# Kernel tuning notes

Measured on AMD Instinct MI355X. Metric: run time of the kernel, lower is better.

## Reference

```python
import jax, jax.numpy as jnp
import numpy as np

T, B, I, H = 512, 128, 512, 1024


def setup_inputs() -> dict:
    key = jax.random.key(0)
    ks = jax.random.split(key, 9)
    stdv = 1.0 / np.sqrt(H).astype(np.float32)
    u = lambda k, shape: jax.random.uniform(k, shape, jnp.float32, -stdv, stdv)
    return {
        "x": jax.random.normal(ks[0], (T, B, I), jnp.float32),
        "Wf": u(ks[1], (H, H + I)), "bf": u(ks[2], (H,)),
        "Wi": u(ks[3], (H, H + I)), "bi": u(ks[4], (H,)),
        "Wc": u(ks[5], (H, H + I)), "bc": u(ks[6], (H,)),
        "Wo": u(ks[7], (H, H + I)), "bo": u(ks[8], (H,)),
    }


def reference(x, Wf, bf, Wi, bi, Wc, bc, Wo, bo):
    # Single-layer unidirectional LSTM (colah equations), scan over time.
    hidden = Wf.shape[0]
    batch = x.shape[1]

    def step(carry, xt):
        h, c = carry
        z = jnp.concatenate([h, xt], axis=-1)          # (B, H+I)
        f = jax.nn.sigmoid(z @ Wf.T + bf)              # forget gate
        i = jax.nn.sigmoid(z @ Wi.T + bi)              # input gate
        c_tilde = jnp.tanh(z @ Wc.T + bc)              # candidate cell
        o = jax.nn.sigmoid(z @ Wo.T + bo)              # output gate
        c_new = f * c + i * c_tilde
        h_new = o * jnp.tanh(c_new)
        return (h_new, c_new), h_new

    h0 = jnp.zeros((batch, hidden), x.dtype)
    c0 = jnp.zeros((batch, hidden), x.dtype)
    (_, _), hs = jax.lax.scan(step, (h0, c0), x)       # hs: (T, B, H)
    return hs
```

## Files before the change

### kernel.cpp

```cpp
#include <hip/hip_runtime.h>
#include <hip/hip_fp16.h>

#define TSTEPS 512
#define NB 128
#define NI 512
#define HID 1024
#define NWGS 256

typedef _Float16 __attribute__((ext_vector_type(8))) half8;
typedef float __attribute__((ext_vector_type(16))) floatx16;
typedef float __attribute__((ext_vector_type(4))) float4v;
typedef unsigned __attribute__((ext_vector_type(4))) uint4v;

#define WPACK_OFF 0
#define HB0_OFF   12582912
#define HB1_OFF   12845056
#define BAR_OFF   13107200

#define LDS_PBUF  98304
#define LDS_HSH   135168
#define LDS_TOTAL 137728

__device__ __forceinline__ short f2h(float f) {
  _Float16 h = (_Float16)f;
  return *reinterpret_cast<short*>(&h);
}

__device__ __forceinline__ half8 pack8(float4v a, float4v b) {
  half8 r;
  r[0] = (_Float16)a[0]; r[1] = (_Float16)a[1]; r[2] = (_Float16)a[2]; r[3] = (_Float16)a[3];
  r[4] = (_Float16)b[0]; r[5] = (_Float16)b[1]; r[6] = (_Float16)b[2]; r[7] = (_Float16)b[3];
  return r;
}

__device__ __forceinline__ float sigf(float x) { return 1.f / (1.f + __expf(-x)); }

__device__ __forceinline__ uint4v cp_load4(const unsigned* p) {
  uint4v v;
  asm volatile("global_load_dwordx4 %0, %1, off sc0 sc1" : "=v"(v) : "v"(p) : "memory");
  asm volatile("s_waitcnt vmcnt(0)" ::: "memory");
  return v;
}
__device__ __forceinline__ void cp_store(unsigned* p, unsigned v) {
  asm volatile("global_store_dword %0, %1, off sc0 sc1" :: "v"(p), "v"(v) : "memory");
}

__global__ void pack_w(const float* __restrict__ Wf, const float* __restrict__ Wi,
                       const float* __restrict__ Wc, const float* __restrict__ Wo,
                       _Float16* __restrict__ wpack) {
  int idx = blockIdx.x * 256 + threadIdx.x;
  if (idx >= 128 * 96 * 64) return;
  int lane = idx & 63;
  int rest = idx >> 6;
  int kt = rest % 96;
  int hs = rest / 96;
  int n = lane & 31, q = lane >> 5;
  int j = n >> 2, g = n & 3;
  int row = hs * 8 + j;
  int k = kt * 16 + q * 8;
  const float* W = (g == 0) ? Wf : (g == 1) ? Wi : (g == 2) ? Wc : Wo;
  const float* src = W + (size_t)row * 1536 + k;
  _Float16* dst = wpack + (size_t)idx * 8;
  #pragma unroll
  for (int e = 0; e < 8; e++) dst[e] = (_Float16)src[e];
}

__global__ void zero_h(unsigned* __restrict__ hb0, unsigned* __restrict__ bar) {
  int i = blockIdx.x * 256 + threadIdx.x;
  if (i < 65536)
    __hip_atomic_store(&hb0[i], 0u, __ATOMIC_RELAXED, __HIP_MEMORY_SCOPE_SYSTEM);
  if (i < 512)
    __hip_atomic_store(&bar[i], 0u, __ATOMIC_RELAXED, __HIP_MEMORY_SCOPE_SYSTEM);
}

__global__ void __launch_bounds__(256, 1)
lstm_main(const float* __restrict__ x,
          const float* __restrict__ bfv, const float* __restrict__ biv,
          const float* __restrict__ bcv, const float* __restrict__ bov,
          const _Float16* __restrict__ wpack,
          _Float16* __restrict__ hb0, _Float16* __restrict__ hb1,
          unsigned* __restrict__ bar, float* __restrict__ out) {
  extern __shared__ char lds[];
  short* wlds = (short*)lds;
  float* pbuf = (float*)(lds + LDS_PBUF);
  float* hshare = (float*)(lds + LDS_HSH);

  const int tid = threadIdx.x;
  const int lane = tid & 63;
  const int wv = tid >> 6;
  const int hs = blockIdx.x & 127;
  const int mh = blockIdx.x >> 7;

  {
    const uint4* src = (const uint4*)wpack + (size_t)hs * 6144;
    uint4* dst = (uint4*)wlds;
    #pragma unroll
    for (int i = 0; i < 24; i++) dst[i * 256 + tid] = src[i * 256 + tid];
  }

  const int rj = tid & 7;
  const int rm4 = tid >> 3;
  float rbias[4] = {0.f, 0.f, 0.f, 0.f};
  float cstate[4] = {0.f, 0.f, 0.f, 0.f};
  if (tid < 128) {
    int hg = hs * 8 + rj;
    rbias[0] = bfv[hg]; rbias[1] = biv[hg]; rbias[2] = bcv[hg]; rbias[3] = bov[hg];
  }

  const int n32 = lane & 31;
  const int q = lane >> 5;

  __syncthreads();

  for (int t = 0; t < TSTEPS; t++) {
    const _Float16* hrd = (t & 1) ? hb1 : hb0;
    _Float16* hwr = (t & 1) ? hb0 : hb1;

    floatx16 acc0, acc1;
    #pragma unroll
    for (int i = 0; i < 16; i++) { acc0[i] = 0.f; acc1[i] = 0.f; }

    {
      const float* xbase = x + (size_t)t * NB * NI;
      const int r0 = (mh * 2 + 0) * 32 + n32;
      #pragma unroll
      for (int kk = 0; kk < 8; kk++) {
        int xt = wv * 8 + kk;
        half8 bfrag = *(const half8*)(wlds + ((64 + xt) * 64 + lane) * 8);
        const float* xs = xbase + xt * 16 + q * 8;
        float4v xa0 = *(const float4v*)(xs + (size_t)r0 * NI);
        float4v xb0 = *(const float4v*)(xs + (size_t)r0 * NI + 4);
        float4v xa1 = *(const float4v*)(xs + (size_t)(r0 + 32) * NI);
        float4v xb1 = *(const float4v*)(xs + (size_t)(r0 + 32) * NI + 4);
        acc0 = __builtin_amdgcn_mfma_f32_32x32x16_f16(pack8(xa0, xb0), bfrag, acc0, 0, 0, 0);
        acc1 = __builtin_amdgcn_mfma_f32_32x32x16_f16(pack8(xa1, xb1), bfrag, acc1, 0, 0, 0);
      }
    }

    if (t > 0) {
      const unsigned need = (unsigned)t;
      if (tid < 32) {
        const unsigned* p = bar + mh * 128 + tid * 4;
        for (;;) {
          uint4v v = cp_load4(p);
          int ok = (v[0] >= need) & (v[1] >= need) & (v[2] >= need) & (v[3] >= need);
          unsigned long long b = __ballot(ok);
          if ((unsigned)b == 0xFFFFFFFFu) break;
          __builtin_amdgcn_s_sleep(2);
        }
      }
      __syncthreads();
    }

    {
      const char* hp = (const char*)hrd + ((size_t)mh << 17);
      #pragma unroll
      for (int ph = 0; ph < 2; ph++) {
        uint4v wa[8], wb[8];
        #pragma unroll
        for (int kk = 0; kk < 8; kk++) {
          int ht = wv * 16 + ph * 8 + kk;
          const char* base = hp + (((ht * 2 + q) << 10) | (n32 << 4));
          asm volatile("global_load_dwordx4 %0, %1, off sc0 sc1"
                       : "=v"(wa[kk]) : "v"(base));
          asm volatile("global_load_dwordx4 %0, %1, off offset:512 sc0 sc1"
                       : "=v"(wb[kk]) : "v"(base));
        }
        #pragma unroll
        for (int kk = 0; kk < 8; kk++) {
          int ht = wv * 16 + ph * 8 + kk;
          half8 bfrag = *(const half8*)(wlds + (ht * 64 + lane) * 8);
          asm volatile("s_waitcnt vmcnt(%0)" :: "i"(14 - 2 * kk) : "memory");
          __builtin_amdgcn_sched_barrier(0);
          union { uint4v u; half8 h; } ua, ub;
          ua.u = wa[kk]; ub.u = wb[kk];
          acc0 = __builtin_amdgcn_mfma_f32_32x32x16_f16(ua.h, bfrag, acc0, 0, 0, 0);
          acc1 = __builtin_amdgcn_mfma_f32_32x32x16_f16(ub.h, bfrag, acc1, 0, 0, 0);
        }
      }
    }

    {
      float* b0 = pbuf + ((wv * 2 + 0) * 32 + n32) * 36 + q * 4;
      float* b1 = pbuf + ((wv * 2 + 1) * 32 + n32) * 36 + q * 4;
      #pragma unroll
      for (int rg = 0; rg < 4; rg++) {
        float4v v0 = {acc0[rg * 4 + 0], acc0[rg * 4 + 1], acc0[rg * 4 + 2], acc0[rg * 4 + 3]};
        float4v v1 = {acc1[rg * 4 + 0], acc1[rg * 4 + 1], acc1[rg * 4 + 2], acc1[rg * 4 + 3]};
        *(float4v*)(b0 + rg * 8) = v0;
        *(float4v*)(b1 + rg * 8) = v1;
      }
    }
    __syncthreads();

    if (tid < 128) {
      const int mt = rm4 >> 3;
      const int mb = (rm4 & 7) * 4;
      float4v s[4];
      #pragma unroll
      for (int g = 0; g < 4; g++) {
        const float* p = pbuf + (mt * 32 + rj * 4 + g) * 36 + mb;
        float4v a = *(const float4v*)(p);
        a += *(const float4v*)(p + 1 * 2 * 32 * 36);
        a += *(const float4v*)(p + 2 * 2 * 32 * 36);
        a += *(const float4v*)(p + 3 * 2 * 32 * 36);
        s[g] = a;
      }
      #pragma unroll
      for (int r = 0; r < 4; r++) {
        float fg = sigf(s[0][r] + rbias[0]);
        float ig = sigf(s[1][r] + rbias[1]);
        float cg = tanhf(s[2][r] + rbias[2]);
        float og = sigf(s[3][r] + rbias[3]);
        float cn = fg * cstate[r] + ig * cg;
        cstate[r] = cn;
        hshare[(rm4 * 4 + r) * 10 + rj] = og * tanhf(cn);
      }
    }
    __syncthreads();

    {
      const int ml = tid >> 2;
      const int j0 = (tid & 3) * 2;
      float h0 = hshare[ml * 10 + j0];
      float h1 = hshare[ml * 10 + j0 + 1];

      unsigned u = ((unsigned)(unsigned short)f2h(h1) << 16) | (unsigned)(unsigned short)f2h(h0);
      unsigned* dst = (unsigned*)((char*)hwr + (((mh * 128 + hs) << 10))) + tid;
      cp_store(dst, u);

      const int mg = mh * 64 + ml;
      const int hg = hs * 8 + j0;
      *(float2*)(out + ((size_t)t * NB + mg) * HID + hg) = make_float2(h0, h1);
    }

    if (t < TSTEPS - 1) {
      __syncthreads();
      if (tid == 0) {
        asm volatile("s_waitcnt vmcnt(0)" ::: "memory");
        cp_store(&bar[blockIdx.x], (unsigned)(t + 1));
      }
    }
  }
}

extern "C" void kernel_launch(void* const* d_in, const int* in_sizes, int n_in,
                              void* d_out, int out_size, void* d_ws, size_t ws_size,
                              hipStream_t stream) {
  const float* x   = (const float*)d_in[0];
  const float* Wf  = (const float*)d_in[1];
  const float* bf_ = (const float*)d_in[2];
  const float* Wi  = (const float*)d_in[3];
  const float* bi_ = (const float*)d_in[4];
  const float* Wc  = (const float*)d_in[5];
  const float* bc_ = (const float*)d_in[6];
  const float* Wo  = (const float*)d_in[7];
  const float* bo_ = (const float*)d_in[8];
  float* out = (float*)d_out;

  char* ws = (char*)d_ws;
  _Float16* wpack = (_Float16*)(ws + WPACK_OFF);
  _Float16* hb0   = (_Float16*)(ws + HB0_OFF);
  _Float16* hb1   = (_Float16*)(ws + HB1_OFF);
  unsigned* bar   = (unsigned*)(ws + BAR_OFF);

  pack_w<<<3072, 256, 0, stream>>>(Wf, Wi, Wc, Wo, wpack);
  zero_h<<<257, 256, 0, stream>>>((unsigned*)hb0, bar);

  hipFuncSetAttribute(reinterpret_cast<const void*>(lstm_main),
                      hipFuncAttributeMaxDynamicSharedMemorySize, LDS_TOTAL);

  void* args[] = {(void*)&x, (void*)&bf_, (void*)&bi_, (void*)&bc_, (void*)&bo_,
                  (void*)&wpack, (void*)&hb0, (void*)&hb1, (void*)&bar, (void*)&out};
  hipLaunchCooperativeKernel(reinterpret_cast<void*>(lstm_main),
                             dim3(NWGS), dim3(256), args, LDS_TOTAL, stream);
}
```

Before: 4.210 ms.

## Drop LDS h staging, skip zero-h matmul at t=0, defer output stores

The gate-math threads now pair adjacent hidden values with a lane shuffle and write the fp16 recurrent state straight to global memory. This removes the LDS hshare buffer and one workgroup barrier per timestep. The h-recurrent MFMA pass now runs only for t>0, so the kernel no longer needs to zero the initial h buffer. The fp32 output stores are issued after the barrier flag is published, so they overlap with other workgroups' waiting. The explicit vmcnt wait before the flag store is gone, so correctness now depends on the barrier's memory fence ordering the h stores before the flag.

```diff
diff --git a/kernel.cpp b/kernel.cpp
--- a/kernel.cpp
+++ b/kernel.cpp
@@ -18,8 +18,7 @@
 #define BAR_OFF   13107200
 
 #define LDS_PBUF  98304
-#define LDS_HSH   135168
-#define LDS_TOTAL 137728
+#define LDS_TOTAL 135168
 
 __device__ __forceinline__ short f2h(float f) {
   _Float16 h = (_Float16)f;
@@ -65,10 +64,8 @@
   for (int e = 0; e < 8; e++) dst[e] = (_Float16)src[e];
 }
 
-__global__ void zero_h(unsigned* __restrict__ hb0, unsigned* __restrict__ bar) {
+__global__ void zero_bar(unsigned* __restrict__ bar) {
   int i = blockIdx.x * 256 + threadIdx.x;
-  if (i < 65536)
-    __hip_atomic_store(&hb0[i], 0u, __ATOMIC_RELAXED, __HIP_MEMORY_SCOPE_SYSTEM);
   if (i < 512)
     __hip_atomic_store(&bar[i], 0u, __ATOMIC_RELAXED, __HIP_MEMORY_SCOPE_SYSTEM);
 }
@@ -83,7 +80,6 @@
   extern __shared__ char lds[];
   short* wlds = (short*)lds;
   float* pbuf = (float*)(lds + LDS_PBUF);
-  float* hshare = (float*)(lds + LDS_HSH);
 
   const int tid = threadIdx.x;
   const int lane = tid & 63;
@@ -150,9 +146,7 @@
         }
       }
       __syncthreads();
-    }
-
-    {
+
       const char* hp = (const char*)hrd + ((size_t)mh << 17);
       #pragma unroll
       for (int ph = 0; ph < 2; ph++) {
@@ -193,6 +187,7 @@
     }
     __syncthreads();
 
+    float hr_keep[4], hp_keep[4];
     if (tid < 128) {
       const int mt = rm4 >> 3;
       const int mb = (rm4 & 7) * 4;
@@ -206,6 +201,7 @@
         a += *(const float4v*)(p + 3 * 2 * 32 * 36);
         s[g] = a;
       }
+      unsigned* hblk = (unsigned*)((char*)hwr + ((mh * 128 + hs) << 10));
       #pragma unroll
       for (int r = 0; r < 4; r++) {
         float fg = sigf(s[0][r] + rbias[0]);
@@ -214,32 +210,30 @@
         float og = sigf(s[3][r] + rbias[3]);
         float cn = fg * cstate[r] + ig * cg;
         cstate[r] = cn;
-        hshare[(rm4 * 4 + r) * 10 + rj] = og * tanhf(cn);
-      }
-    }
-    __syncthreads();
-
-    {
-      const int ml = tid >> 2;
-      const int j0 = (tid & 3) * 2;
-      float h0 = hshare[ml * 10 + j0];
-      float h1 = hshare[ml * 10 + j0 + 1];
-
-      unsigned u = ((unsigned)(unsigned short)f2h(h1) << 16) | (unsigned)(unsigned short)f2h(h0);
-      unsigned* dst = (unsigned*)((char*)hwr + (((mh * 128 + hs) << 10))) + tid;
-      cp_store(dst, u);
-
-      const int mg = mh * 64 + ml;
-      const int hg = hs * 8 + j0;
-      *(float2*)(out + ((size_t)t * NB + mg) * HID + hg) = make_float2(h0, h1);
+        float hv = og * tanhf(cn);
+        float hpart = __shfl_xor(hv, 1, 64);
+        hr_keep[r] = hv; hp_keep[r] = hpart;
+        if ((rj & 1) == 0) {
+          unsigned u = ((unsigned)(unsigned short)f2h(hpart) << 16)
+                     | (unsigned)(unsigned short)f2h(hv);
+          cp_store(hblk + ((rm4 * 4 + r) * 4 + (rj >> 1)), u);
+        }
+      }
     }
 
     if (t < TSTEPS - 1) {
       __syncthreads();
-      if (tid == 0) {
-        asm volatile("s_waitcnt vmcnt(0)" ::: "memory");
-        cp_store(&bar[blockIdx.x], (unsigned)(t + 1));
-      }
+      if (tid == 0) cp_store(&bar[blockIdx.x], (unsigned)(t + 1));
+    } else {
+      __syncthreads();
+    }
+
+    if (tid < 128 && (rj & 1) == 0) {
+      const int mgb = mh * 64 + rm4 * 4;
+      float* ob = out + ((size_t)t * NB + mgb) * HID + hs * 8 + rj;
+      #pragma unroll
+      for (int r = 0; r < 4; r++)
+        *(float2*)(ob + (size_t)r * HID) = make_float2(hr_keep[r], hp_keep[r]);
     }
   }
 }
@@ -265,7 +259,7 @@
   unsigned* bar   = (unsigned*)(ws + BAR_OFF);
 
   pack_w<<<3072, 256, 0, stream>>>(Wf, Wi, Wc, Wo, wpack);
-  zero_h<<<257, 256, 0, stream>>>((unsigned*)hb0, bar);
+  zero_bar<<<2, 256, 0, stream>>>(bar);
 
   hipFuncSetAttribute(reinterpret_cast<const void*>(lstm_main),
                       hipFuncAttributeMaxDynamicSharedMemorySize, LDS_TOTAL);
```

Result: slower. 4.338 ms (+3.1%).
